# Optimization experiments

Measured on AMD Instinct MI355X. Metric: run time of the kernel, lower is better.

## Reference

```python
import jax, jax.numpy as jnp
import numpy as np

N = 128                      # reduced state dimension (Q_dim[0])
S = N * (N + 1) // 2         # number of triu pairwise products = 8256
BATCH = 16384                # snapshot columns
_rows, _cols = np.triu_indices(N)
ROWS = jnp.asarray(_rows)    # [S] int32 constants
COLS = jnp.asarray(_cols)


def setup_inputs() -> dict:
    key = jax.random.key(0)
    kx, ka, kb = jax.random.split(key, 3)
    x = jax.random.normal(kx, (N, BATCH), dtype=jnp.float32)
    # learned operators (module inits them to zeros; use small random for a meaningful baseline)
    A = jax.random.normal(ka, (N, N), dtype=jnp.float32) * 0.02
    B = jax.random.normal(kb, (N, S), dtype=jnp.float32) * 0.02
    return {"x": x, "A": A, "B": B}


def reference(x, A, B):
    # quadratic feature expansion: x2[k, :] = x[i_k, :] * x[j_k, :] over triu pairs
    x2 = x[ROWS] * x[COLS]                 # [S, BATCH]
    return A @ x + B @ x2                  # [N, BATCH]
```

## Files before the change

### kernel.cpp

```cpp
#include <hip/hip_runtime.h>


constexpr int N_     = 128;
constexpr int S_     = 8256;
constexpr int BATCH_ = 16384;
constexpr int KTOT   = 8384;
constexpr int NKT    = 131;
constexpr int LD     = 136;
constexpr size_t WT_BYTES = (size_t)KTOT * 128 * 2;
constexpr size_t PP_OFF   = WT_BYTES;

typedef __attribute__((ext_vector_type(8))) short short8;
typedef __attribute__((ext_vector_type(4))) float f32x4;
typedef __attribute__((ext_vector_type(2))) float f32x2;

__device__ __forceinline__ float bf2f(ushort h) {
    unsigned u = (unsigned)h << 16;
    float f;
    __builtin_memcpy(&f, &u, 4);
    return f;
}
__device__ __forceinline__ ushort f2bf(float f) {
    unsigned u;
    __builtin_memcpy(&u, &f, 4);
    u = (u + 0x7FFFu + ((u >> 16) & 1u)) >> 16;
    return (ushort)u;
}
__device__ __forceinline__ uint fbits(float f) {
    uint u; __builtin_memcpy(&u, &f, 4); return u;
}

__global__ void build_perm(ushort* __restrict__ pp) {
    int i = threadIdx.x;
    if (i >= 128) return;
    pp[i] = (ushort)(i | (0xFFu << 8));
    int off_n = 0, off_r = 0;
    for (int q = 0; q < i; ++q) {
        off_n += 16 - ((q + 7) >> 3);
        off_r += (8 - (q & 7)) & 7;
    }
    const int jb0 = (i + 7) >> 3;
    const int kb = 128 + off_n * 8;
    for (int jb = jb0; jb < 16; ++jb) {
        const int j0 = jb * 8;
        for (int e = 0; e < 8; ++e)
            pp[kb + (jb - jb0) * 8 + e] = (ushort)(i | ((j0 + e) << 8));
    }
    const int h = (8 - (i & 7)) & 7;
    const int rb = 7936 + off_r;
    for (int e = 0; e < h; ++e)
        pp[rb + e] = (ushort)(i | ((i + e) << 8));
}

__global__ void build_wt(const float* __restrict__ A, const float* __restrict__ B,
                         const ushort* __restrict__ pp, ushort* __restrict__ wt) {
    int e  = blockIdx.x * 256 + threadIdx.x;
    int kt = e >> 13;
    int r  = e & 8191;
    int kk = r >> 12;
    int wmm = (r >> 11) & 1;
    int mt = (r >> 9) & 3;
    int lane = (r >> 3) & 63;
    int el = r & 7;
    int m  = wmm * 64 + mt * 16 + (lane & 15);
    int k  = kt * 64 + kk * 32 + (lane >> 4) * 8 + el;
    uint pr = pp[k];
    uint i = pr & 0xFFu, j = pr >> 8;
    float v;
    if (j == 0xFFu) v = A[m * 128 + i];
    else {
        int s = (int)(i * (257 - i) / 2 + (j - i));
        v = B[(size_t)m * S_ + s];
    }
    wt[e] = f2bf(v);
}

__device__ __forceinline__ void load_af(short8 af[8], const ushort* __restrict__ wt,
                                        int kt, int wm, int lane) {
    const ushort* ab = wt + ((size_t)kt << 13) + (wm << 11) + (lane << 3);
    #pragma unroll
    for (int kk = 0; kk < 2; ++kk)
        #pragma unroll
        for (int mt = 0; mt < 4; ++mt)
            af[kk * 4 + mt] = *(const short8*)(ab + (kk << 12) + (mt << 9));
}

__device__ __forceinline__ void step_nice(f32x4 acc[4][2], const short8 af[8],
                                          uint prc, const ushort* __restrict__ xr0,
                                          const ushort* __restrict__ xr1) {
    const uint i0a = prc & 0xFFu, j0a = (prc >> 8) & 0xFFu;
    const uint i0b = (prc >> 16) & 0xFFu, j0b = prc >> 24;
    const ushort xia0 = xr0[i0a], xia1 = xr1[i0a];
    const ushort xib0 = xr0[i0b], xib1 = xr1[i0b];
    uint wa0[4], wa1[4], wb0[4], wb1[4];
    __builtin_memcpy(wa0, xr0 + j0a, 16);
    __builtin_memcpy(wa1, xr1 + j0a, 16);
    __builtin_memcpy(wb0, xr0 + j0b, 16);
    __builtin_memcpy(wb1, xr1 + j0b, 16);

    short8 bfr[2][2];
    #pragma unroll
    for (int v = 0; v < 4; ++v) {
        const uint*  wsx = (v == 0) ? wa0 : (v == 1) ? wa1 : (v == 2) ? wb0 : wb1;
        const ushort xis = (v == 0) ? xia0 : (v == 1) ? xia1 : (v == 2) ? xib0 : xib1;
        const float xi = bf2f(xis);
        const f32x2 xi2 = {xi, xi};
        uint ow[4];
        #pragma unroll
        for (int p = 0; p < 4; ++p) {
            const uint lo = wsx[p] << 16;
            const uint hi = wsx[p] & 0xFFFF0000u;
            f32x2 a;
            { float fl, fh;
              __builtin_memcpy(&fl, &lo, 4);
              __builtin_memcpy(&fh, &hi, 4);
              a.x = fl; a.y = fh; }
            const f32x2 o = a * xi2;
            ow[p] = __builtin_amdgcn_perm(fbits(o.y), fbits(o.x),
                                          0x07060302u);
        }
        __builtin_memcpy(&bfr[v >> 1][v & 1], ow, 16);
    }
    #pragma unroll
    for (int kk = 0; kk < 2; ++kk)
        #pragma unroll
        for (int mt = 0; mt < 4; ++mt)
            #pragma unroll
            for (int nt = 0; nt < 2; ++nt)
                acc[mt][nt] = __builtin_amdgcn_mfma_f32_16x16x32_bf16(
                    af[kk * 4 + mt], bfr[kk][nt], acc[mt][nt], 0, 0, 0);
}

__global__ __launch_bounds__(512) void gemm_mfma(
    const float*  __restrict__ x,
    const ushort* __restrict__ wt,
    const ushort* __restrict__ pp,
    float* __restrict__ out)
{
    __shared__ ushort xt[128 * LD];
    __shared__ uint   ppc[NKT * 4];

    const int t    = threadIdx.x;
    const int b0   = blockIdx.x * 128;
    const int sp   = blockIdx.y;
    const int kt0  = sp ? 66 : 0;
    const int kt1  = sp ? NKT : 66;
    const int lane = t & 63;
    const int w    = t >> 6;
    const int wm   = w >> 2, wn = w & 3;
    const int l16  = lane & 15, quad = lane >> 4;

    {
        const int n = t & 127, g = t >> 7;
        #pragma unroll
        for (int c = 0; c < 4; ++c) {
            const int rb = g * 32 + c * 8;
            uint ow[4];
            #pragma unroll
            for (int p = 0; p < 4; ++p) {
                const ushort u0 = f2bf(x[(size_t)(rb + 2 * p) * BATCH_ + b0 + n]);
                const ushort u1 = f2bf(x[(size_t)(rb + 2 * p + 1) * BATCH_ + b0 + n]);
                ow[p] = (uint)u0 | ((uint)u1 << 16);
            }
            __builtin_memcpy(&xt[n * LD + rb], ow, 16);
        }
    }
    for (int idx = t; idx < NKT * 4; idx += 512) {
        const int kt = idx >> 2, q = idx & 3;
        const uint w0 = *(const uint*)(pp + kt * 64 + q * 8);
        const uint w1 = *(const uint*)(pp + kt * 64 + 32 + q * 8);
        ppc[idx] = (w0 & 0xFFFFu) | ((w1 & 0xFFFFu) << 16);
    }
    __syncthreads();

    f32x4 acc[4][2];
    #pragma unroll
    for (int mt = 0; mt < 4; ++mt)
        #pragma unroll
        for (int nt = 0; nt < 2; ++nt)
            acc[mt][nt] = (f32x4){0.f, 0.f, 0.f, 0.f};

    const ushort* xr0 = xt + (wn * 32 + l16) * LD;
    const ushort* xr1 = xr0 + 16 * LD;

    if (sp == 0) {
        for (int kt = 0; kt < 2; ++kt) {
            short8 af[8];
            load_af(af, wt, kt, wm, lane);
            short8 bfr[2][2];
            #pragma unroll
            for (int kk = 0; kk < 2; ++kk) {
                const int off = kt * 64 + kk * 32 + quad * 8;
                bfr[kk][0] = *(const short8*)(xr0 + off);
                bfr[kk][1] = *(const short8*)(xr1 + off);
            }
            #pragma unroll
            for (int kk = 0; kk < 2; ++kk)
                #pragma unroll
                for (int mt = 0; mt < 4; ++mt)
                    #pragma unroll
                    for (int nt = 0; nt < 2; ++nt)
                        acc[mt][nt] = __builtin_amdgcn_mfma_f32_16x16x32_bf16(
                            af[kk * 4 + mt], bfr[kk][nt], acc[mt][nt], 0, 0, 0);
        }
    }

    {
        const int s_ni = (kt0 > 2) ? kt0 : 2;
        const int e_ni = (kt1 < 124) ? kt1 : 124;
        int kt = s_ni;
        if (kt < e_ni) {
            short8 afA[8], afB[8];
            load_af(afA, wt, kt, wm, lane);
            uint prc = ppc[kt * 4 + quad];
            while (true) {
                {
                    const int ktn = (kt + 1 < e_ni) ? kt + 1 : kt;
                    load_af(afB, wt, ktn, wm, lane);
                    const uint prn = ppc[ktn * 4 + quad];
                    step_nice(acc, afA, prc, xr0, xr1);
                    prc = prn; ++kt;
                }
                if (kt >= e_ni) break;
                {
                    const int ktn = (kt + 1 < e_ni) ? kt + 1 : kt;
                    load_af(afA, wt, ktn, wm, lane);
                    const uint prn = ppc[ktn * 4 + quad];
                    step_nice(acc, afB, prc, xr0, xr1);
                    prc = prn; ++kt;
                }
                if (kt >= e_ni) break;
            }
        }
    }

    if (sp == 1) {
        for (int kt = 124; kt < NKT; ++kt) {
            short8 af[8];
            load_af(af, wt, kt, wm, lane);
            short8 bfr[2][2];
            #pragma unroll
            for (int kk = 0; kk < 2; ++kk) {
                const int k0 = kt * 64 + kk * 32 + quad * 8;
                const uint4 pk = *(const uint4*)(pp + k0);
                const uint pr4[4] = {pk.x, pk.y, pk.z, pk.w};
                #pragma unroll
                for (int nt = 0; nt < 2; ++nt) {
                    const ushort* xr = nt ? xr1 : xr0;
                    float prods[8];
                    #pragma unroll
                    for (int e = 0; e < 8; ++e) {
                        const uint ent = (pr4[e >> 1] >> ((e & 1) * 16)) & 0xFFFFu;
                        prods[e] = bf2f(xr[ent & 0xFFu]) * bf2f(xr[ent >> 8]);
                    }
                    uint ow[4];
                    #pragma unroll
                    for (int p = 0; p < 4; ++p)
                        ow[p] = __builtin_amdgcn_perm(fbits(prods[2 * p + 1]),
                                                      fbits(prods[2 * p]),
                                                      0x07060302u);
                    __builtin_memcpy(&bfr[kk][nt], ow, 16);
                }
            }
            #pragma unroll
            for (int kk = 0; kk < 2; ++kk)
                #pragma unroll
                for (int mt = 0; mt < 4; ++mt)
                    #pragma unroll
                    for (int nt = 0; nt < 2; ++nt)
                        acc[mt][nt] = __builtin_amdgcn_mfma_f32_16x16x32_bf16(
                            af[kk * 4 + mt], bfr[kk][nt], acc[mt][nt], 0, 0, 0);
        }
    }

    #pragma unroll
    for (int mt = 0; mt < 4; ++mt) {
        #pragma unroll
        for (int nt = 0; nt < 2; ++nt) {
            const int mbase = wm * 64 + mt * 16 + quad * 4;
            const size_t col = (size_t)b0 + wn * 32 + nt * 16 + l16;
            #pragma unroll
            for (int r = 0; r < 4; ++r)
                unsafeAtomicAdd(&out[(size_t)(mbase + r) * BATCH_ + col],
                                acc[mt][nt][r]);
        }
    }
}

extern "C" void kernel_launch(void* const* d_in, const int* in_sizes, int n_in,
                              void* d_out, int out_size, void* d_ws, size_t ws_size,
                              hipStream_t stream) {
    const float* x = (const float*)d_in[0];
    const float* A = (const float*)d_in[1];
    const float* B = (const float*)d_in[2];
    float* out = (float*)d_out;

    ushort* wt = (ushort*)d_ws;
    ushort* pp = (ushort*)((char*)d_ws + PP_OFF);

    hipMemsetAsync(out, 0, (size_t)N_ * BATCH_ * sizeof(float), stream);
    build_perm<<<1, 128, 0, stream>>>(pp);
    build_wt<<<4192, 256, 0, stream>>>(A, B, pp, wt);
    gemm_mfma<<<dim3(BATCH_ / 128, 2), 512, 0, stream>>>(x, wt, pp, out);
}
```

Baseline: 126.6 us.

## Fuse prep kernels, compute pair indices analytically, split K four ways

Removes the permutation-table kernel and the memset by computing the (i,j) pair for each K index in closed form, then folds output zeroing and weight packing into one prep kernel. The GEMM grid's K split grows from 2 to 4 partitions, giving twice as many blocks and shorter K loops per block. In exchange there are more atomic adds to the output, and index arithmetic is recomputed on the fly instead of read from a table.

```diff
diff --git a/kernel.cpp b/kernel.cpp
--- a/kernel.cpp
+++ b/kernel.cpp
@@ -8,7 +8,6 @@
 constexpr int NKT    = 131;
 constexpr int LD     = 136;
 constexpr size_t WT_BYTES = (size_t)KTOT * 128 * 2;
-constexpr size_t PP_OFF   = WT_BYTES;
 
 typedef __attribute__((ext_vector_type(8))) short short8;
 typedef __attribute__((ext_vector_type(4))) float f32x4;
@@ -30,49 +29,64 @@
     uint u; __builtin_memcpy(&u, &f, 4); return u;
 }
 
-__global__ void build_perm(ushort* __restrict__ pp) {
-    int i = threadIdx.x;
-    if (i >= 128) return;
-    pp[i] = (ushort)(i | (0xFFu << 8));
-    int off_n = 0, off_r = 0;
-    for (int q = 0; q < i; ++q) {
-        off_n += 16 - ((q + 7) >> 3);
-        off_r += (8 - (q & 7)) & 7;
-    }
-    const int jb0 = (i + 7) >> 3;
-    const int kb = 128 + off_n * 8;
-    for (int jb = jb0; jb < 16; ++jb) {
-        const int j0 = jb * 8;
-        for (int e = 0; e < 8; ++e)
-            pp[kb + (jb - jb0) * 8 + e] = (ushort)(i | ((j0 + e) << 8));
-    }
-    const int h = (8 - (i & 7)) & 7;
-    const int rb = 7936 + off_r;
-    for (int e = 0; e < h; ++e)
-        pp[rb + e] = (ushort)(i | ((i + e) << 8));
-}
-
-__global__ void build_wt(const float* __restrict__ A, const float* __restrict__ B,
-                         const ushort* __restrict__ pp, ushort* __restrict__ wt) {
-    int e  = blockIdx.x * 256 + threadIdx.x;
-    int kt = e >> 13;
-    int r  = e & 8191;
-    int kk = r >> 12;
-    int wmm = (r >> 11) & 1;
-    int mt = (r >> 9) & 3;
-    int lane = (r >> 3) & 63;
-    int el = r & 7;
-    int m  = wmm * 64 + mt * 16 + (lane & 15);
-    int k  = kt * 64 + kk * 32 + (lane >> 4) * 8 + el;
-    uint pr = pp[k];
-    uint i = pr & 0xFFu, j = pr >> 8;
-    float v;
-    if (j == 0xFFu) v = A[m * 128 + i];
-    else {
-        int s = (int)(i * (257 - i) / 2 + (j - i));
-        v = B[(size_t)m * S_ + s];
-    }
-    wt[e] = f2bf(v);
+__device__ __forceinline__ uint nice_octet(int o) {
+    float f = sqrtf(9.0f + 16.0f * (float)o);
+    int jb = (int)((3.0f + f) * 0.125f);
+    while (jb * (4 * jb - 3) > o) --jb;
+    while ((jb + 1) * (4 * jb + 1) <= o) ++jb;
+    const int i = o - jb * (4 * jb - 3);
+    return (uint)i | ((uint)(jb << 3) << 8);
+}
+
+__device__ __forceinline__ uint rag_pair(int c) {
+    const int blk = c / 28, rem = c - blk * 28;
+    int r, tb;
+    if      (rem >= 27) { r = 7; tb = 27; }
+    else if (rem >= 25) { r = 6; tb = 25; }
+    else if (rem >= 22) { r = 5; tb = 22; }
+    else if (rem >= 18) { r = 4; tb = 18; }
+    else if (rem >= 13) { r = 3; tb = 13; }
+    else if (rem >= 7)  { r = 2; tb = 7;  }
+    else                { r = 1; tb = 0;  }
+    const int i = blk * 8 + r;
+    const int j = i + (rem - tb);
+    return (uint)i | ((uint)j << 8);
+}
+
+__device__ __forceinline__ float w_value(const float* __restrict__ A,
+                                         const float* __restrict__ B,
+                                         int m, int k) {
+    if (k < 128) return A[m * 128 + k];
+    uint p;
+    if (k < 7936) {
+        p = nice_octet((k - 128) >> 3);
+        p += (uint)(k & 7) << 8;
+    } else {
+        p = rag_pair(k - 7936);
+    }
+    const int i = (int)(p & 0xFFu), j = (int)(p >> 8);
+    const int s = i * (257 - i) / 2 + (j - i);
+    return B[(size_t)m * S_ + s];
+}
+
+__global__ void prep(const float* __restrict__ A, const float* __restrict__ B,
+                     ushort* __restrict__ wt, float* __restrict__ out) {
+    const int b = blockIdx.x;
+    if (b < 2048) {
+        ((float4*)out)[b * 256 + threadIdx.x] = make_float4(0.f, 0.f, 0.f, 0.f);
+        return;
+    }
+    const int e  = (b - 2048) * 256 + threadIdx.x;
+    const int kt = e >> 13;
+    const int r  = e & 8191;
+    const int kk = r >> 12;
+    const int wmm = (r >> 11) & 1;
+    const int mt = (r >> 9) & 3;
+    const int lane = (r >> 3) & 63;
+    const int el = r & 7;
+    const int m  = wmm * 64 + mt * 16 + (lane & 15);
+    const int k  = kt * 64 + kk * 32 + (lane >> 4) * 8 + el;
+    wt[e] = f2bf(w_value(A, B, m, k));
 }
 
 __device__ __forceinline__ void load_af(short8 af[8], const ushort* __restrict__ wt,
@@ -134,7 +148,6 @@
 __global__ __launch_bounds__(512) void gemm_mfma(
     const float*  __restrict__ x,
     const ushort* __restrict__ wt,
-    const ushort* __restrict__ pp,
     float* __restrict__ out)
 {
     __shared__ ushort xt[128 * LD];
@@ -143,8 +156,8 @@
     const int t    = threadIdx.x;
     const int b0   = blockIdx.x * 128;
     const int sp   = blockIdx.y;
-    const int kt0  = sp ? 66 : 0;
-    const int kt1  = sp ? NKT : 66;
+    const int kt0  = sp * 33;
+    const int kt1  = (sp == 3) ? NKT : kt0 + 33;
     const int lane = t & 63;
     const int w    = t >> 6;
     const int wm   = w >> 2, wn = w & 3;
@@ -167,9 +180,14 @@
     }
     for (int idx = t; idx < NKT * 4; idx += 512) {
         const int kt = idx >> 2, q = idx & 3;
-        const uint w0 = *(const uint*)(pp + kt * 64 + q * 8);
-        const uint w1 = *(const uint*)(pp + kt * 64 + 32 + q * 8);
-        ppc[idx] = (w0 & 0xFFFFu) | ((w1 & 0xFFFFu) << 16);
+        uint v = 0;
+        const int k0 = kt * 64 + q * 8;
+        if (k0 >= 128 && k0 + 32 < 7936) {
+            const uint a = nice_octet((k0 - 128) >> 3);
+            const uint b = nice_octet((k0 + 32 - 128) >> 3);
+            v = a | (b << 16);
+        }
+        ppc[idx] = v;
     }
     __syncthreads();
 
@@ -234,25 +252,24 @@
         }
     }
 
-    if (sp == 1) {
+    if (sp == 3) {
         for (int kt = 124; kt < NKT; ++kt) {
             short8 af[8];
             load_af(af, wt, kt, wm, lane);
             short8 bfr[2][2];
             #pragma unroll
             for (int kk = 0; kk < 2; ++kk) {
-                const int k0 = kt * 64 + kk * 32 + quad * 8;
-                const uint4 pk = *(const uint4*)(pp + k0);
-                const uint pr4[4] = {pk.x, pk.y, pk.z, pk.w};
+                const int cb = kt * 64 + kk * 32 + quad * 8 - 7936;
+                uint prs[8];
+                #pragma unroll
+                for (int e = 0; e < 8; ++e) prs[e] = rag_pair(cb + e);
                 #pragma unroll
                 for (int nt = 0; nt < 2; ++nt) {
                     const ushort* xr = nt ? xr1 : xr0;
                     float prods[8];
                     #pragma unroll
-                    for (int e = 0; e < 8; ++e) {
-                        const uint ent = (pr4[e >> 1] >> ((e & 1) * 16)) & 0xFFFFu;
-                        prods[e] = bf2f(xr[ent & 0xFFu]) * bf2f(xr[ent >> 8]);
-                    }
+                    for (int e = 0; e < 8; ++e)
+                        prods[e] = bf2f(xr[prs[e] & 0xFFu]) * bf2f(xr[prs[e] >> 8]);
                     uint ow[4];
                     #pragma unroll
                     for (int p = 0; p < 4; ++p)
@@ -296,10 +313,7 @@
     float* out = (float*)d_out;
 
     ushort* wt = (ushort*)d_ws;
-    ushort* pp = (ushort*)((char*)d_ws + PP_OFF);
-
-    hipMemsetAsync(out, 0, (size_t)N_ * BATCH_ * sizeof(float), stream);
-    build_perm<<<1, 128, 0, stream>>>(pp);
-    build_wt<<<4192, 256, 0, stream>>>(A, B, pp, wt);
-    gemm_mfma<<<dim3(BATCH_ / 128, 2), 512, 0, stream>>>(x, wt, pp, out);
-}
+
+    prep<<<2048 + 4192, 256, 0, stream>>>(A, B, wt, out);
+    gemm_mfma<<<dim3(BATCH_ / 128, 4), 512, 0, stream>>>(x, wt, out);
+}
```

Result: slower. 133.8 us (+5.7%).
